# Performance work log

Hardware: AMD Instinct MI355X
Metric: run time of the kernel (lower is better)

Reference implementation:

```python
import jax, jax.numpy as jnp
import numpy as np

IN_DIM = 256
QK_DIM = IN_DIM // 8


def setup_inputs() -> dict:
    key = jax.random.key(0)
    ks = jax.random.split(key, 7)
    B, C, H, W = 4, IN_DIM, 64, 64
    s = 0.05
    return {
        "x": jax.random.normal(ks[0], (B, C, H, W), dtype=jnp.float32),
        "Wq": jax.random.normal(ks[1], (QK_DIM, C), dtype=jnp.float32) * s,
        "bq": jnp.zeros((QK_DIM,), dtype=jnp.float32),
        "Wk": jax.random.normal(ks[2], (QK_DIM, C), dtype=jnp.float32) * s,
        "bk": jnp.zeros((QK_DIM,), dtype=jnp.float32),
        "Wv": jax.random.normal(ks[3], (C, C), dtype=jnp.float32) * s,
        "bv": jnp.zeros((C,), dtype=jnp.float32),
        "gamma": jnp.zeros((1,), dtype=jnp.float32),
    }


def reference(x, Wq, bq, Wk, bk, Wv, bv, gamma):
    B, C, H, W = x.shape
    N = H * W
    xf = x.reshape(B, C, N)  # [B, C, N]
    # 1x1 convs are channel matmuls
    q = jnp.einsum('oc,bcn->bno', Wq, xf) + bq  # [B, N, Cqk]
    k = jnp.einsum('oc,bcn->bon', Wk, xf) + bk[None, :, None]  # [B, Cqk, N]
    energy = jnp.einsum('bno,bom->bnm', q, k)  # [B, N, N]
    attn = jax.nn.softmax(energy, axis=-1)
    v = jnp.einsum('oc,bcn->bon', Wv, xf) + bv[None, :, None]  # [B, C, N]
    # torch: out = bmm(v, attn^T) -> out[b,c,m] = sum_n v[b,c,n]*attn[m,n]
    out = jnp.einsum('bcn,bmn->bcm', v, attn)
    out = out.reshape(B, C, H, W)
    return gamma[0] * out + x
```

## Files before the change

kernel.cpp:

```cpp
#include <hip/hip_runtime.h>
#include <hip/hip_bf16.h>
#include <cstddef>

#define NB  4
#define NC  256
#define NN  4096
#define DQK 32
#define MT  64
#define JT  64
#define NIT (NN / JT)
#define PSTR 72
#define XSTR 40

typedef __attribute__((ext_vector_type(8))) short short8;
typedef __attribute__((ext_vector_type(4))) float f32x4;

#define MFMA16(a, b, c) __builtin_amdgcn_mfma_f32_16x16x32_bf16((a), (b), (c), 0, 0, 0)

__device__ inline unsigned pk2bf(float a, float b) {
  __hip_bfloat162 h = __float22bfloat162_rn(make_float2(a, b));
  unsigned u;
  __builtin_memcpy(&u, &h, 4);
  return u;
}

__global__ __launch_bounds__(256) void wcvt_kernel(
    const float* __restrict__ Wq, const float* __restrict__ Wk,
    const float* __restrict__ Wv, __hip_bfloat16* __restrict__ W16) {
  const int id4 = (blockIdx.x * 256 + threadIdx.x) * 4;
  const int row = id4 >> 8, col = id4 & 255;
  const float* src = (row < 32) ? Wq + row * 256
                   : (row < 64) ? Wk + (row - 32) * 256
                                : Wv + (row - 64) * 256;
  float4 vv = *(const float4*)(src + col);
  *(uint2*)(W16 + id4) = make_uint2(pk2bf(vv.x, vv.y), pk2bf(vv.z, vv.w));
}

__global__ __launch_bounds__(256) void proj_kernel(
    const float* __restrict__ x, const __hip_bfloat16* __restrict__ W16,
    const float* __restrict__ bq, const float* __restrict__ bk,
    const float* __restrict__ bv, __hip_bfloat16* __restrict__ q,
    __hip_bfloat16* __restrict__ kT, __hip_bfloat16* __restrict__ v) {
  __shared__ __hip_bfloat16 Xs[32 * XSTR];
  const int t = threadIdx.x;
  const int b = blockIdx.y, n0 = blockIdx.x * 32;
  const int w = __builtin_amdgcn_readfirstlane(t >> 6);
  const int ln = t & 15, quad = (t & 63) >> 4;
  const int sn = t & 31, scg = t >> 5;

  f32x4 zero4 = {0.f, 0.f, 0.f, 0.f};
  f32x4 acc[5][2];
#pragma unroll
  for (int i = 0; i < 5; ++i)
#pragma unroll
    for (int j = 0; j < 2; ++j) acc[i][j] = zero4;

  const float* xsrc = x + (size_t)b * NC * NN + n0 + sn;
  float xr[4];
#pragma unroll
  for (int i = 0; i < 4; ++i) xr[i] = xsrc[(size_t)(scg * 4 + i) * NN];

  for (int k0 = 0; k0 < NC; k0 += 32) {
    const unsigned px0 = pk2bf(xr[0], xr[1]);
    const unsigned px1 = pk2bf(xr[2], xr[3]);
    __syncthreads();
    *(uint2*)&Xs[sn * XSTR + scg * 4] = make_uint2(px0, px1);
    __syncthreads();
    const int kn = k0 + 32;
    if (kn < NC) {
#pragma unroll
      for (int i = 0; i < 4; ++i) xr[i] = xsrc[(size_t)(kn + scg * 4 + i) * NN];
    }
    short8 af[5], bfr[2];
#pragma unroll
    for (int ot = 0; ot < 5; ++ot)
      af[ot] = *(const short8*)(W16 + (size_t)(w * 80 + ot * 16 + ln) * NC + k0 + quad * 8);
#pragma unroll
    for (int nt = 0; nt < 2; ++nt)
      bfr[nt] = *(const short8*)&Xs[(nt * 16 + ln) * XSTR + quad * 8];
#pragma unroll
    for (int ot = 0; ot < 5; ++ot)
#pragma unroll
      for (int nt = 0; nt < 2; ++nt)
        acc[ot][nt] = MFMA16(af[ot], bfr[nt], acc[ot][nt]);
  }

#pragma unroll
  for (int ot = 0; ot < 5; ++ot) {
    const int gbase = w * 80 + ot * 16;
    if (gbase < 32) {
#pragma unroll
      for (int nt = 0; nt < 2; ++nt)
#pragma unroll
        for (int r = 0; r < 4; ++r) {
          const int row = gbase + quad * 4 + r;
          q[((size_t)b * NN + n0 + nt * 16 + ln) * DQK + row] =
              __hip_bfloat16(acc[ot][nt][r] + bq[row]);
        }
    } else if (gbase < 64) {
#pragma unroll
      for (int nt = 0; nt < 2; ++nt)
#pragma unroll
        for (int r = 0; r < 4; ++r) {
          const int row = gbase - 32 + quad * 4 + r;
          kT[((size_t)b * NN + n0 + nt * 16 + ln) * DQK + row] =
              __hip_bfloat16(acc[ot][nt][r] + bk[row]);
        }
    } else {
#pragma unroll
      for (int nt = 0; nt < 2; ++nt)
#pragma unroll
        for (int r = 0; r < 4; ++r) {
          const int c = gbase - 64 + quad * 4 + r;
          v[((size_t)b * NC + c) * NN + n0 + nt * 16 + ln] =
              __hip_bfloat16(acc[ot][nt][r] + bv[c]);
        }
    }
  }
}

__global__ __launch_bounds__(512, 2) void flash_kernel(
    const __hip_bfloat16* __restrict__ q, const __hip_bfloat16* __restrict__ kt,
    const __hip_bfloat16* __restrict__ v, const float* __restrict__ x,
    const float* __restrict__ gamma, float* __restrict__ out) {
  __shared__ __hip_bfloat16 Ps[2][MT * PSTR];
  __shared__ float arow[2][MT];
  __shared__ float lrow[MT];

  const int t  = threadIdx.x;
  const int bi = blockIdx.x;
  const int b  = (bi & 7) >> 1;
  const int m0 = (((bi & 1) * 32) + (bi >> 3)) * MT;

  const int w    = __builtin_amdgcn_readfirstlane(t >> 6);
  const int ln   = t & 15;
  const int quad = (t & 63) >> 4;

  const __hip_bfloat16* kb_base = kt + (size_t)b * NN * DQK;
  const __hip_bfloat16* v_base  = v + (size_t)b * NC * NN;

  if (w < 4) {
    const short8 qa =
        *(const short8*)(q + ((size_t)b * NN + m0 + w * 16 + ln) * DQK + quad * 8);
    float mreg[4], lreg[4];
#pragma unroll
    for (int r = 0; r < 4; ++r) { mreg[r] = -3.0e38f; lreg[r] = 0.f; }

    f32x4 zero4 = {0.f, 0.f, 0.f, 0.f};
    short8 kb[4];
#pragma unroll
    for (int jt = 0; jt < 4; ++jt)
      kb[jt] = *(const short8*)(kb_base + (size_t)(jt * 16 + ln) * DQK + quad * 8);

    for (int it = 0; it < NIT; ++it) {
      f32x4 sf[4];
#pragma unroll
      for (int jt = 0; jt < 4; ++jt) sf[jt] = MFMA16(qa, kb[jt], zero4);

      if (it + 1 < NIT) {
        const int jn = (it + 1) * JT;
#pragma unroll
        for (int jt = 0; jt < 4; ++jt)
          kb[jt] = *(const short8*)(kb_base + (size_t)(jn + jt * 16 + ln) * DQK + quad * 8);
      }

      float rmax[4];
#pragma unroll
      for (int r = 0; r < 4; ++r)
        rmax[r] = fmaxf(fmaxf(sf[0][r], sf[1][r]), fmaxf(sf[2][r], sf[3][r]));
#pragma unroll
      for (int off = 1; off < 16; off <<= 1)
#pragma unroll
        for (int r = 0; r < 4; ++r)
          rmax[r] = fmaxf(rmax[r], __shfl_xor(rmax[r], off));
      float alpha[4];
#pragma unroll
      for (int r = 0; r < 4; ++r) {
        const float mn = fmaxf(mreg[r], rmax[r]);
        alpha[r] = __expf(mreg[r] - mn);
        mreg[r] = mn;
      }
      float e[4][4], rsum[4];
#pragma unroll
      for (int r = 0; r < 4; ++r) rsum[r] = 0.f;
#pragma unroll
      for (int jt = 0; jt < 4; ++jt)
#pragma unroll
        for (int r = 0; r < 4; ++r) {
          e[jt][r] = __expf(sf[jt][r] - mreg[r]);
          rsum[r] += e[jt][r];
        }
#pragma unroll
      for (int off = 1; off < 16; off <<= 1)
#pragma unroll
        for (int r = 0; r < 4; ++r) rsum[r] += __shfl_xor(rsum[r], off);
#pragma unroll
      for (int r = 0; r < 4; ++r) lreg[r] = lreg[r] * alpha[r] + rsum[r];

      const int buf = it & 1;
#pragma unroll
      for (int jt = 0; jt < 4; ++jt)
#pragma unroll
        for (int r = 0; r < 4; ++r)
          Ps[buf][(w * 16 + quad * 4 + r) * PSTR + jt * 16 + ln] = __hip_bfloat16(e[jt][r]);
      if (ln == 0) {
#pragma unroll
        for (int r = 0; r < 4; ++r) arow[buf][w * 16 + quad * 4 + r] = alpha[r];
      }
      __syncthreads();
    }
    if (ln == 0) {
#pragma unroll
      for (int r = 0; r < 4; ++r) lrow[w * 16 + quad * 4 + r] = lreg[r];
    }
    __syncthreads();
  } else {
    const int c0 = (w - 4) * 64;
    f32x4 zero4 = {0.f, 0.f, 0.f, 0.f};
    f32x4 acc[4][4];
#pragma unroll
    for (int ct = 0; ct < 4; ++ct)
#pragma unroll
      for (int mt = 0; mt < 4; ++mt) acc[ct][mt] = zero4;

    short8 va[4][2];
#pragma unroll
    for (int ct = 0; ct < 4; ++ct)
#pragma unroll
      for (int ks = 0; ks < 2; ++ks)
        va[ct][ks] = *(const short8*)(v_base +
            (size_t)(c0 + ct * 16 + ln) * NN + ks * 32 + quad * 8);
    __syncthreads();

    for (int it = 1; it < NIT; ++it) {
      const int pbuf = (it - 1) & 1;
      float av[4];
#pragma unroll
      for (int mt = 0; mt < 4; ++mt) av[mt] = arow[pbuf][mt * 16 + ln];
#pragma unroll
      for (int ct = 0; ct < 4; ++ct)
#pragma unroll
        for (int mt = 0; mt < 4; ++mt) acc[ct][mt] *= av[mt];

#pragma unroll
      for (int ks = 0; ks < 2; ++ks) {
        short8 pb[4];
#pragma unroll
        for (int mt = 0; mt < 4; ++mt)
          pb[mt] = *(const short8*)&Ps[pbuf][(mt * 16 + ln) * PSTR + ks * 32 + quad * 8];
#pragma unroll
        for (int ct = 0; ct < 4; ++ct)
#pragma unroll
          for (int mt = 0; mt < 4; ++mt)
            acc[ct][mt] = MFMA16(va[ct][ks], pb[mt], acc[ct][mt]);
      }

      const int j0 = it * JT;
#pragma unroll
      for (int ct = 0; ct < 4; ++ct)
#pragma unroll
        for (int ks = 0; ks < 2; ++ks)
          va[ct][ks] = *(const short8*)(v_base +
              (size_t)(c0 + ct * 16 + ln) * NN + j0 + ks * 32 + quad * 8);
      __syncthreads();
    }

    {
      const int pbuf = (NIT - 1) & 1;
      float av[4];
#pragma unroll
      for (int mt = 0; mt < 4; ++mt) av[mt] = arow[pbuf][mt * 16 + ln];
#pragma unroll
      for (int ct = 0; ct < 4; ++ct)
#pragma unroll
        for (int mt = 0; mt < 4; ++mt) acc[ct][mt] *= av[mt];
#pragma unroll
      for (int ks = 0; ks < 2; ++ks) {
        short8 pb[4];
#pragma unroll
        for (int mt = 0; mt < 4; ++mt)
          pb[mt] = *(const short8*)&Ps[pbuf][(mt * 16 + ln) * PSTR + ks * 32 + quad * 8];
#pragma unroll
        for (int ct = 0; ct < 4; ++ct)
#pragma unroll
          for (int mt = 0; mt < 4; ++mt)
            acc[ct][mt] = MFMA16(va[ct][ks], pb[mt], acc[ct][mt]);
      }
    }
    __syncthreads();

    const float g0 = gamma[0];
    float li[4];
#pragma unroll
    for (int mt = 0; mt < 4; ++mt) li[mt] = 1.f / lrow[mt * 16 + ln];
#pragma unroll
    for (int ct = 0; ct < 4; ++ct)
#pragma unroll
      for (int r = 0; r < 4; ++r) {
        const int c = c0 + ct * 16 + quad * 4 + r;
        const float* xr = x + ((size_t)b * NC + c) * NN + m0;
        float* orow = out + ((size_t)b * NC + c) * NN + m0;
#pragma unroll
        for (int mt = 0; mt < 4; ++mt) {
          const int m = mt * 16 + ln;
          orow[m] = g0 * (acc[ct][mt][r] * li[mt]) + xr[m];
        }
      }
  }
}

extern "C" void kernel_launch(void* const* d_in, const int* in_sizes, int n_in,
                              void* d_out, int out_size, void* d_ws, size_t ws_size,
                              hipStream_t stream) {
  const float* x     = (const float*)d_in[0];
  const float* Wq    = (const float*)d_in[1];
  const float* bq    = (const float*)d_in[2];
  const float* Wk    = (const float*)d_in[3];
  const float* bk    = (const float*)d_in[4];
  const float* Wv    = (const float*)d_in[5];
  const float* bv    = (const float*)d_in[6];
  const float* gamma = (const float*)d_in[7];
  float* out = (float*)d_out;

  char* wsp = (char*)d_ws;
  __hip_bfloat16* W16 = (__hip_bfloat16*)wsp;  wsp += (size_t)320 * NC * 2;
  __hip_bfloat16* q   = (__hip_bfloat16*)wsp;  wsp += (size_t)NB * NN * DQK * 2;
  __hip_bfloat16* kT  = (__hip_bfloat16*)wsp;  wsp += (size_t)NB * NN * DQK * 2;
  __hip_bfloat16* v   = (__hip_bfloat16*)wsp;

  wcvt_kernel<<<dim3(80), dim3(256), 0, stream>>>(Wq, Wk, Wv, W16);
  proj_kernel<<<dim3(NN / 32, NB), dim3(256), 0, stream>>>(x, W16, bq, bk, bv, q, kT, v);
  flash_kernel<<<dim3(NB * NN / MT), dim3(512), 0, stream>>>(q, kT, v, x, gamma, out);
}
```

Before: 170.2 us.

## Halve flash query tile and replace MFMA projection with scalar fp32 kernels

Shrinks the flash-attention query tile from 64 to 32 rows and drops the block to 256 threads, with 2 softmax waves and 2 PV waves that each own 128 channels. This doubles the number of blocks, and each block now re-reads the full K and V for half as many queries. The bf16 weight-conversion kernel and the MFMA-based projection kernel are replaced by two scalar fp32 kernels, one for Q/K and one for V, which read the weights directly. The change trades projection-stage tensor-core use and V/K reuse for more parallelism in the attention stage.

Result: slower. 323.5 us (+90.1%).

```diff
diff --git a/kernel.cpp b/kernel.cpp
--- a/kernel.cpp
+++ b/kernel.cpp
@@ -6,11 +6,10 @@
 #define NC  256
 #define NN  4096
 #define DQK 32
-#define MT  64
+#define MT  32
 #define JT  64
 #define NIT (NN / JT)
 #define PSTR 72
-#define XSTR 40
 
 typedef __attribute__((ext_vector_type(8))) short short8;
 typedef __attribute__((ext_vector_type(4))) float f32x4;
@@ -24,102 +23,64 @@
   return u;
 }
 
-__global__ __launch_bounds__(256) void wcvt_kernel(
-    const float* __restrict__ Wq, const float* __restrict__ Wk,
-    const float* __restrict__ Wv, __hip_bfloat16* __restrict__ W16) {
-  const int id4 = (blockIdx.x * 256 + threadIdx.x) * 4;
-  const int row = id4 >> 8, col = id4 & 255;
-  const float* src = (row < 32) ? Wq + row * 256
-                   : (row < 64) ? Wk + (row - 32) * 256
-                                : Wv + (row - 64) * 256;
-  float4 vv = *(const float4*)(src + col);
-  *(uint2*)(W16 + id4) = make_uint2(pk2bf(vv.x, vv.y), pk2bf(vv.z, vv.w));
-}
-
-__global__ __launch_bounds__(256) void proj_kernel(
-    const float* __restrict__ x, const __hip_bfloat16* __restrict__ W16,
-    const float* __restrict__ bq, const float* __restrict__ bk,
-    const float* __restrict__ bv, __hip_bfloat16* __restrict__ q,
-    __hip_bfloat16* __restrict__ kT, __hip_bfloat16* __restrict__ v) {
-  __shared__ __hip_bfloat16 Xs[32 * XSTR];
+__global__ __launch_bounds__(256) void proj_qk_kernel(
+    const float* __restrict__ x, const float* __restrict__ Wq,
+    const float* __restrict__ bq, const float* __restrict__ Wk,
+    const float* __restrict__ bk, __hip_bfloat16* __restrict__ q,
+    __hip_bfloat16* __restrict__ kT) {
   const int t = threadIdx.x;
-  const int b = blockIdx.y, n0 = blockIdx.x * 32;
-  const int w = __builtin_amdgcn_readfirstlane(t >> 6);
-  const int ln = t & 15, quad = (t & 63) >> 4;
-  const int sn = t & 31, scg = t >> 5;
-
-  f32x4 zero4 = {0.f, 0.f, 0.f, 0.f};
-  f32x4 acc[5][2];
-#pragma unroll
-  for (int i = 0; i < 5; ++i)
-#pragma unroll
-    for (int j = 0; j < 2; ++j) acc[i][j] = zero4;
-
-  const float* xsrc = x + (size_t)b * NC * NN + n0 + sn;
-  float xr[4];
-#pragma unroll
-  for (int i = 0; i < 4; ++i) xr[i] = xsrc[(size_t)(scg * 4 + i) * NN];
-
-  for (int k0 = 0; k0 < NC; k0 += 32) {
-    const unsigned px0 = pk2bf(xr[0], xr[1]);
-    const unsigned px1 = pk2bf(xr[2], xr[3]);
-    __syncthreads();
-    *(uint2*)&Xs[sn * XSTR + scg * 4] = make_uint2(px0, px1);
-    __syncthreads();
-    const int kn = k0 + 32;
-    if (kn < NC) {
-#pragma unroll
-      for (int i = 0; i < 4; ++i) xr[i] = xsrc[(size_t)(kn + scg * 4 + i) * NN];
-    }
-    short8 af[5], bfr[2];
-#pragma unroll
-    for (int ot = 0; ot < 5; ++ot)
-      af[ot] = *(const short8*)(W16 + (size_t)(w * 80 + ot * 16 + ln) * NC + k0 + quad * 8);
-#pragma unroll
-    for (int nt = 0; nt < 2; ++nt)
-      bfr[nt] = *(const short8*)&Xs[(nt * 16 + ln) * XSTR + quad * 8];
-#pragma unroll
-    for (int ot = 0; ot < 5; ++ot)
-#pragma unroll
-      for (int nt = 0; nt < 2; ++nt)
-        acc[ot][nt] = MFMA16(af[ot], bfr[nt], acc[ot][nt]);
+  const int b = blockIdx.y;
+  const int n = blockIdx.x * 64 + (t & 63);
+  const int g = __builtin_amdgcn_readfirstlane(t >> 6);
+  const float* W    = (g < 2) ? Wq : Wk;
+  const float* bias = (g < 2) ? bq : bk;
+  const int obase = (g & 1) * 16;
+
+  float acc[16];
+#pragma unroll
+  for (int i = 0; i < 16; ++i) acc[i] = bias[obase + i];
+
+  const float* xp = x + ((size_t)b * NC) * NN + n;
+#pragma unroll 4
+  for (int c = 0; c < NC; ++c) {
+    float xv = xp[(size_t)c * NN];
+#pragma unroll
+    for (int i = 0; i < 16; ++i) acc[i] += W[(obase + i) * NC + c] * xv;
   }
-
-#pragma unroll
-  for (int ot = 0; ot < 5; ++ot) {
-    const int gbase = w * 80 + ot * 16;
-    if (gbase < 32) {
-#pragma unroll
-      for (int nt = 0; nt < 2; ++nt)
-#pragma unroll
-        for (int r = 0; r < 4; ++r) {
-          const int row = gbase + quad * 4 + r;
-          q[((size_t)b * NN + n0 + nt * 16 + ln) * DQK + row] =
-              __hip_bfloat16(acc[ot][nt][r] + bq[row]);
-        }
-    } else if (gbase < 64) {
-#pragma unroll
-      for (int nt = 0; nt < 2; ++nt)
-#pragma unroll
-        for (int r = 0; r < 4; ++r) {
-          const int row = gbase - 32 + quad * 4 + r;
-          kT[((size_t)b * NN + n0 + nt * 16 + ln) * DQK + row] =
-              __hip_bfloat16(acc[ot][nt][r] + bk[row]);
-        }
-    } else {
-#pragma unroll
-      for (int nt = 0; nt < 2; ++nt)
-#pragma unroll
-        for (int r = 0; r < 4; ++r) {
-          const int c = gbase - 64 + quad * 4 + r;
-          v[((size_t)b * NC + c) * NN + n0 + nt * 16 + ln] =
-              __hip_bfloat16(acc[ot][nt][r] + bv[c]);
-        }
-    }
+  __hip_bfloat16* dst = ((g < 2) ? q : kT) + ((size_t)b * NN + n) * DQK + obase;
+  unsigned p[8];
+#pragma unroll
+  for (int i = 0; i < 8; ++i) p[i] = pk2bf(acc[2 * i], acc[2 * i + 1]);
+  ((uint4*)dst)[0] = make_uint4(p[0], p[1], p[2], p[3]);
+  ((uint4*)dst)[1] = make_uint4(p[4], p[5], p[6], p[7]);
+}
+
+__global__ __launch_bounds__(256) void proj_v_kernel(
+    const float* __restrict__ x, const float* __restrict__ Wv,
+    const float* __restrict__ bv, __hip_bfloat16* __restrict__ v) {
+  const int t = threadIdx.x;
+  const int b = blockIdx.z;
+  const int n = blockIdx.x * 64 + (t & 63);
+  const int g = __builtin_amdgcn_readfirstlane(t >> 6);
+  const int obase = blockIdx.y * 128 + g * 32;
+
+  float acc[32];
+#pragma unroll
+  for (int i = 0; i < 32; ++i) acc[i] = bv[obase + i];
+
+  const float* xp = x + ((size_t)b * NC) * NN + n;
+#pragma unroll 2
+  for (int c = 0; c < NC; ++c) {
+    float xv = xp[(size_t)c * NN];
+#pragma unroll
+    for (int i = 0; i < 32; ++i) acc[i] += Wv[(obase + i) * NC + c] * xv;
   }
-}
-
-__global__ __launch_bounds__(512, 2) void flash_kernel(
+#pragma unroll
+  for (int i = 0; i < 32; ++i)
+    v[((size_t)b * NC + obase + i) * NN + n] = __hip_bfloat16(acc[i]);
+}
+
+__global__ __launch_bounds__(256, 2) void flash_kernel(
     const __hip_bfloat16* __restrict__ q, const __hip_bfloat16* __restrict__ kt,
     const __hip_bfloat16* __restrict__ v, const float* __restrict__ x,
     const float* __restrict__ gamma, float* __restrict__ out) {
@@ -130,7 +91,7 @@
   const int t  = threadIdx.x;
   const int bi = blockIdx.x;
   const int b  = (bi & 7) >> 1;
-  const int m0 = (((bi & 1) * 32) + (bi >> 3)) * MT;
+  const int m0 = (((bi & 1) * 64) + (bi >> 3)) * MT;
 
   const int w    = __builtin_amdgcn_readfirstlane(t >> 6);
   const int ln   = t & 15;
@@ -139,7 +100,7 @@
   const __hip_bfloat16* kb_base = kt + (size_t)b * NN * DQK;
   const __hip_bfloat16* v_base  = v + (size_t)b * NC * NN;
 
-  if (w < 4) {
+  if (w < 2) {
     const short8 qa =
         *(const short8*)(q + ((size_t)b * NN + m0 + w * 16 + ln) * DQK + quad * 8);
     float mreg[4], lreg[4];
@@ -215,17 +176,17 @@
     }
     __syncthreads();
   } else {
-    const int c0 = (w - 4) * 64;
+    const int c0 = (w - 2) * 128;
     f32x4 zero4 = {0.f, 0.f, 0.f, 0.f};
-    f32x4 acc[4][4];
-#pragma unroll
-    for (int ct = 0; ct < 4; ++ct)
-#pragma unroll
-      for (int mt = 0; mt < 4; ++mt) acc[ct][mt] = zero4;
-
-    short8 va[4][2];
-#pragma unroll
-    for (int ct = 0; ct < 4; ++ct)
+    f32x4 acc[8][2];
+#pragma unroll
+    for (int ct = 0; ct < 8; ++ct)
+#pragma unroll
+      for (int mt = 0; mt < 2; ++mt) acc[ct][mt] = zero4;
+
+    short8 va[8][2];
+#pragma unroll
+    for (int ct = 0; ct < 8; ++ct)
 #pragma unroll
       for (int ks = 0; ks < 2; ++ks)
         va[ct][ks] = *(const short8*)(v_base +
@@ -234,30 +195,30 @@
 
     for (int it = 1; it < NIT; ++it) {
       const int pbuf = (it - 1) & 1;
-      float av[4];
-#pragma unroll
-      for (int mt = 0; mt < 4; ++mt) av[mt] = arow[pbuf][mt * 16 + ln];
-#pragma unroll
-      for (int ct = 0; ct < 4; ++ct)
-#pragma unroll
-        for (int mt = 0; mt < 4; ++mt) acc[ct][mt] *= av[mt];
+      float av[2];
+#pragma unroll
+      for (int mt = 0; mt < 2; ++mt) av[mt] = arow[pbuf][mt * 16 + ln];
+#pragma unroll
+      for (int ct = 0; ct < 8; ++ct)
+#pragma unroll
+        for (int mt = 0; mt < 2; ++mt) acc[ct][mt] *= av[mt];
 
 #pragma unroll
       for (int ks = 0; ks < 2; ++ks) {
-        short8 pb[4];
-#pragma unroll
-        for (int mt = 0; mt < 4; ++mt)
+        short8 pb[2];
+#pragma unroll
+        for (int mt = 0; mt < 2; ++mt)
           pb[mt] = *(const short8*)&Ps[pbuf][(mt * 16 + ln) * PSTR + ks * 32 + quad * 8];
 #pragma unroll
-        for (int ct = 0; ct < 4; ++ct)
-#pragma unroll
-          for (int mt = 0; mt < 4; ++mt)
+        for (int ct = 0; ct < 8; ++ct)
+#pragma unroll
+          for (int mt = 0; mt < 2; ++mt)
             acc[ct][mt] = MFMA16(va[ct][ks], pb[mt], acc[ct][mt]);
       }
 
       const int j0 = it * JT;
 #pragma unroll
-      for (int ct = 0; ct < 4; ++ct)
+      for (int ct = 0; ct < 8; ++ct)
 #pragma unroll
         for (int ks = 0; ks < 2; ++ks)
           va[ct][ks] = *(const short8*)(v_base +
@@ -267,41 +228,41 @@
 
     {
       const int pbuf = (NIT - 1) & 1;
-      float av[4];
-#pragma unroll
-      for (int mt = 0; mt < 4; ++mt) av[mt] = arow[pbuf][mt * 16 + ln];
-#pragma unroll
-      for (int ct = 0; ct < 4; ++ct)
-#pragma unroll
-        for (int mt = 0; mt < 4; ++mt) acc[ct][mt] *= av[mt];
+      float av[2];
+#pragma unroll
+      for (int mt = 0; mt < 2; ++mt) av[mt] = arow[pbuf][mt * 16 + ln];
+#pragma unroll
+      for (int ct = 0; ct < 8; ++ct)
+#pragma unroll
+        for (int mt = 0; mt < 2; ++mt) acc[ct][mt] *= av[mt];
 #pragma unroll
       for (int ks = 0; ks < 2; ++ks) {
-        short8 pb[4];
-#pragma unroll
-        for (int mt = 0; mt < 4; ++mt)
+        short8 pb[2];
+#pragma unroll
+        for (int mt = 0; mt < 2; ++mt)
           pb[mt] = *(const short8*)&Ps[pbuf][(mt * 16 + ln) * PSTR + ks * 32 + quad * 8];
 #pragma unroll
-        for (int ct = 0; ct < 4; ++ct)
-#pragma unroll
-          for (int mt = 0; mt < 4; ++mt)
+        for (int ct = 0; ct < 8; ++ct)
+#pragma unroll
+          for (int mt = 0; mt < 2; ++mt)
             acc[ct][mt] = MFMA16(va[ct][ks], pb[mt], acc[ct][mt]);
       }
     }
     __syncthreads();
 
     const float g0 = gamma[0];
-    float li[4];
-#pragma unroll
-    for (int mt = 0; mt < 4; ++mt) li[mt] = 1.f / lrow[mt * 16 + ln];
-#pragma unroll
-    for (int ct = 0; ct < 4; ++ct)
+    float li[2];
+#pragma unroll
+    for (int mt = 0; mt < 2; ++mt) li[mt] = 1.f / lrow[mt * 16 + ln];
+#pragma unroll
+    for (int ct = 0; ct < 8; ++ct)
 #pragma unroll
       for (int r = 0; r < 4; ++r) {
         const int c = c0 + ct * 16 + quad * 4 + r;
         const float* xr = x + ((size_t)b * NC + c) * NN + m0;
         float* orow = out + ((size_t)b * NC + c) * NN + m0;
 #pragma unroll
-        for (int mt = 0; mt < 4; ++mt) {
+        for (int mt = 0; mt < 2; ++mt) {
           const int m = mt * 16 + ln;
           orow[m] = g0 * (acc[ct][mt][r] * li[mt]) + xr[m];
         }
@@ -322,13 +283,11 @@
   const float* gamma = (const float*)d_in[7];
   float* out = (float*)d_out;
 
-  char* wsp = (char*)d_ws;
-  __hip_bfloat16* W16 = (__hip_bfloat16*)wsp;  wsp += (size_t)320 * NC * 2;
-  __hip_bfloat16* q   = (__hip_bfloat16*)wsp;  wsp += (size_t)NB * NN * DQK * 2;
-  __hip_bfloat16* kT  = (__hip_bfloat16*)wsp;  wsp += (size_t)NB * NN * DQK * 2;
-  __hip_bfloat16* v   = (__hip_bfloat16*)wsp;
-
-  wcvt_kernel<<<dim3(80), dim3(256), 0, stream>>>(Wq, Wk, Wv, W16);
-  proj_kernel<<<dim3(NN / 32, NB), dim3(256), 0, stream>>>(x, W16, bq, bk, bv, q, kT, v);
-  flash_kernel<<<dim3(NB * NN / MT), dim3(512), 0, stream>>>(q, kT, v, x, gamma, out);
-}
+  __hip_bfloat16* q  = (__hip_bfloat16*)d_ws;
+  __hip_bfloat16* kT = q  + (size_t)NB * NN * DQK;
+  __hip_bfloat16* v  = kT + (size_t)NB * NN * DQK;
+
+  proj_qk_kernel<<<dim3(NN / 64, NB), dim3(256), 0, stream>>>(x, Wq, bq, Wk, bk, q, kT);
+  proj_v_kernel<<<dim3(NN / 64, 2, NB), dim3(256), 0, stream>>>(x, Wv, bv, v);
+  flash_kernel<<<dim3(NB * NN / MT), dim3(256), 0, stream>>>(q, kT, v, x, gamma, out);
+}
```

## Replace MFMA projection with fp32 scalar proj kernels and double flash key tile

Applied to the files above, without the earlier changes.

Drops the weight-conversion kernel and the bf16 MFMA projection, replacing them with two fp32 scalar-FMA projection kernels (one for q/k, one for v). Each splits the channel reduction across two wave groups and combines the halves through shared memory. In the flash kernel the key tile grows from 64 to 128, halving the number of iterations and barriers, and V loads are interleaved per k-slice. The trade-off is more registers and shared memory in flash, plus a scalar-FMA projection that may be slower than the MFMA version and rereads x for each output group.

After: 235.9 us. 38.6% more time.

```diff
diff --git a/kernel.cpp b/kernel.cpp
--- a/kernel.cpp
+++ b/kernel.cpp
@@ -7,10 +7,9 @@
 #define NN  4096
 #define DQK 32
 #define MT  64
-#define JT  64
+#define JT  128
 #define NIT (NN / JT)
-#define PSTR 72
-#define XSTR 40
+#define PSTR 140
 
 typedef __attribute__((ext_vector_type(8))) short short8;
 typedef __attribute__((ext_vector_type(4))) float f32x4;
@@ -24,97 +23,112 @@
   return u;
 }
 
-__global__ __launch_bounds__(256) void wcvt_kernel(
-    const float* __restrict__ Wq, const float* __restrict__ Wk,
-    const float* __restrict__ Wv, __hip_bfloat16* __restrict__ W16) {
-  const int id4 = (blockIdx.x * 256 + threadIdx.x) * 4;
-  const int row = id4 >> 8, col = id4 & 255;
-  const float* src = (row < 32) ? Wq + row * 256
-                   : (row < 64) ? Wk + (row - 32) * 256
-                                : Wv + (row - 64) * 256;
-  float4 vv = *(const float4*)(src + col);
-  *(uint2*)(W16 + id4) = make_uint2(pk2bf(vv.x, vv.y), pk2bf(vv.z, vv.w));
-}
-
-__global__ __launch_bounds__(256) void proj_kernel(
-    const float* __restrict__ x, const __hip_bfloat16* __restrict__ W16,
-    const float* __restrict__ bq, const float* __restrict__ bk,
-    const float* __restrict__ bv, __hip_bfloat16* __restrict__ q,
-    __hip_bfloat16* __restrict__ kT, __hip_bfloat16* __restrict__ v) {
-  __shared__ __hip_bfloat16 Xs[32 * XSTR];
+__global__ __launch_bounds__(512) void proj_qk_kernel(
+    const float* __restrict__ x, const float* __restrict__ Wq,
+    const float* __restrict__ bq, const float* __restrict__ Wk,
+    const float* __restrict__ bk, __hip_bfloat16* __restrict__ q,
+    __hip_bfloat16* __restrict__ kT) {
+  __shared__ float Rs[256 * 17];
   const int t = threadIdx.x;
-  const int b = blockIdx.y, n0 = blockIdx.x * 32;
+  const int b = blockIdx.y;
+  const int n = blockIdx.x * 64 + (t & 63);
   const int w = __builtin_amdgcn_readfirstlane(t >> 6);
-  const int ln = t & 15, quad = (t & 63) >> 4;
-  const int sn = t & 31, scg = t >> 5;
-
-  f32x4 zero4 = {0.f, 0.f, 0.f, 0.f};
-  f32x4 acc[5][2];
-#pragma unroll
-  for (int i = 0; i < 5; ++i)
-#pragma unroll
-    for (int j = 0; j < 2; ++j) acc[i][j] = zero4;
-
-  const float* xsrc = x + (size_t)b * NC * NN + n0 + sn;
-  float xr[4];
-#pragma unroll
-  for (int i = 0; i < 4; ++i) xr[i] = xsrc[(size_t)(scg * 4 + i) * NN];
-
-  for (int k0 = 0; k0 < NC; k0 += 32) {
-    const unsigned px0 = pk2bf(xr[0], xr[1]);
-    const unsigned px1 = pk2bf(xr[2], xr[3]);
-    __syncthreads();
-    *(uint2*)&Xs[sn * XSTR + scg * 4] = make_uint2(px0, px1);
-    __syncthreads();
-    const int kn = k0 + 32;
-    if (kn < NC) {
-#pragma unroll
-      for (int i = 0; i < 4; ++i) xr[i] = xsrc[(size_t)(kn + scg * 4 + i) * NN];
-    }
-    short8 af[5], bfr[2];
-#pragma unroll
-    for (int ot = 0; ot < 5; ++ot)
-      af[ot] = *(const short8*)(W16 + (size_t)(w * 80 + ot * 16 + ln) * NC + k0 + quad * 8);
-#pragma unroll
-    for (int nt = 0; nt < 2; ++nt)
-      bfr[nt] = *(const short8*)&Xs[(nt * 16 + ln) * XSTR + quad * 8];
-#pragma unroll
-    for (int ot = 0; ot < 5; ++ot)
-#pragma unroll
-      for (int nt = 0; nt < 2; ++nt)
-        acc[ot][nt] = MFMA16(af[ot], bfr[nt], acc[ot][nt]);
-  }
-
-#pragma unroll
-  for (int ot = 0; ot < 5; ++ot) {
-    const int gbase = w * 80 + ot * 16;
-    if (gbase < 32) {
-#pragma unroll
-      for (int nt = 0; nt < 2; ++nt)
-#pragma unroll
-        for (int r = 0; r < 4; ++r) {
-          const int row = gbase + quad * 4 + r;
-          q[((size_t)b * NN + n0 + nt * 16 + ln) * DQK + row] =
-              __hip_bfloat16(acc[ot][nt][r] + bq[row]);
-        }
-    } else if (gbase < 64) {
-#pragma unroll
-      for (int nt = 0; nt < 2; ++nt)
-#pragma unroll
-        for (int r = 0; r < 4; ++r) {
-          const int row = gbase - 32 + quad * 4 + r;
-          kT[((size_t)b * NN + n0 + nt * 16 + ln) * DQK + row] =
-              __hip_bfloat16(acc[ot][nt][r] + bk[row]);
-        }
-    } else {
-#pragma unroll
-      for (int nt = 0; nt < 2; ++nt)
-#pragma unroll
-        for (int r = 0; r < 4; ++r) {
-          const int c = gbase - 64 + quad * 4 + r;
-          v[((size_t)b * NC + c) * NN + n0 + nt * 16 + ln] =
-              __hip_bfloat16(acc[ot][nt][r] + bv[c]);
-        }
+  const int g = w & 3;
+  const int ch = w >> 2;
+  const float* W    = (g < 2) ? Wq : Wk;
+  const int obase = (g & 1) * 16;
+
+  float acc[16];
+#pragma unroll
+  for (int i = 0; i < 16; ++i) acc[i] = 0.f;
+
+  const float* xp = x + ((size_t)b * NC + ch * 128) * NN + n;
+  const float* Wp = W + obase * NC + ch * 128;
+
+  float xv[8];
+#pragma unroll
+  for (int i = 0; i < 8; ++i) xv[i] = xp[(size_t)i * NN];
+  for (int cc = 0; cc < 128; cc += 8) {
+    float xn[8];
+    if (cc + 8 < 128) {
+#pragma unroll
+      for (int i = 0; i < 8; ++i) xn[i] = xp[(size_t)(cc + 8 + i) * NN];
+    }
+#pragma unroll
+    for (int i = 0; i < 8; ++i)
+#pragma unroll
+      for (int o = 0; o < 16; ++o) acc[o] += Wp[o * NC + cc + i] * xv[i];
+#pragma unroll
+    for (int i = 0; i < 8; ++i) xv[i] = xn[i];
+  }
+
+  if (w >= 4) {
+    const int tl = t - 256;
+#pragma unroll
+    for (int i = 0; i < 16; ++i) Rs[tl * 17 + i] = acc[i];
+  }
+  __syncthreads();
+  if (w < 4) {
+    const float* bias = (g < 2) ? bq : bk;
+#pragma unroll
+    for (int i = 0; i < 16; ++i) acc[i] += Rs[t * 17 + i] + bias[obase + i];
+    __hip_bfloat16* dst = ((g < 2) ? q : kT) + ((size_t)b * NN + n) * DQK + obase;
+    unsigned p[8];
+#pragma unroll
+    for (int i = 0; i < 8; ++i) p[i] = pk2bf(acc[2 * i], acc[2 * i + 1]);
+    ((uint4*)dst)[0] = make_uint4(p[0], p[1], p[2], p[3]);
+    ((uint4*)dst)[1] = make_uint4(p[4], p[5], p[6], p[7]);
+  }
+}
+
+__global__ __launch_bounds__(512) void proj_v_kernel(
+    const float* __restrict__ x, const float* __restrict__ Wv,
+    const float* __restrict__ bv, __hip_bfloat16* __restrict__ v) {
+  __shared__ float Rs[256 * 17];
+  const int t = threadIdx.x;
+  const int b = blockIdx.z;
+  const int n = blockIdx.x * 64 + (t & 63);
+  const int w = __builtin_amdgcn_readfirstlane(t >> 6);
+  const int g = w & 3;
+  const int ch = w >> 2;
+  const int obase = blockIdx.y * 64 + g * 16;
+
+  float acc[16];
+#pragma unroll
+  for (int i = 0; i < 16; ++i) acc[i] = 0.f;
+
+  const float* xp = x + ((size_t)b * NC + ch * 128) * NN + n;
+  const float* Wp = Wv + obase * NC + ch * 128;
+
+  float xv[8];
+#pragma unroll
+  for (int i = 0; i < 8; ++i) xv[i] = xp[(size_t)i * NN];
+  for (int cc = 0; cc < 128; cc += 8) {
+    float xn[8];
+    if (cc + 8 < 128) {
+#pragma unroll
+      for (int i = 0; i < 8; ++i) xn[i] = xp[(size_t)(cc + 8 + i) * NN];
+    }
+#pragma unroll
+    for (int i = 0; i < 8; ++i)
+#pragma unroll
+      for (int o = 0; o < 16; ++o) acc[o] += Wp[o * NC + cc + i] * xv[i];
+#pragma unroll
+    for (int i = 0; i < 8; ++i) xv[i] = xn[i];
+  }
+
+  if (w >= 4) {
+    const int tl = t - 256;
+#pragma unroll
+    for (int i = 0; i < 16; ++i) Rs[tl * 17 + i] = acc[i];
+  }
+  __syncthreads();
+  if (w < 4) {
+#pragma unroll
+    for (int i = 0; i < 16; ++i) {
+      const int c = obase + i;
+      v[((size_t)b * NC + c) * NN + n] =
+          __hip_bfloat16(acc[i] + Rs[t * 17 + i] + bv[c]);
     }
   }
 }
@@ -147,27 +161,30 @@
     for (int r = 0; r < 4; ++r) { mreg[r] = -3.0e38f; lreg[r] = 0.f; }
 
     f32x4 zero4 = {0.f, 0.f, 0.f, 0.f};
-    short8 kb[4];
-#pragma unroll
-    for (int jt = 0; jt < 4; ++jt)
+    short8 kb[8];
+#pragma unroll
+    for (int jt = 0; jt < 8; ++jt)
       kb[jt] = *(const short8*)(kb_base + (size_t)(jt * 16 + ln) * DQK + quad * 8);
 
     for (int it = 0; it < NIT; ++it) {
-      f32x4 sf[4];
-#pragma unroll
-      for (int jt = 0; jt < 4; ++jt) sf[jt] = MFMA16(qa, kb[jt], zero4);
+      f32x4 sf[8];
+#pragma unroll
+      for (int jt = 0; jt < 8; ++jt) sf[jt] = MFMA16(qa, kb[jt], zero4);
 
       if (it + 1 < NIT) {
         const int jn = (it + 1) * JT;
 #pragma unroll
-        for (int jt = 0; jt < 4; ++jt)
+        for (int jt = 0; jt < 8; ++jt)
           kb[jt] = *(const short8*)(kb_base + (size_t)(jn + jt * 16 + ln) * DQK + quad * 8);
       }
 
       float rmax[4];
 #pragma unroll
-      for (int r = 0; r < 4; ++r)
-        rmax[r] = fmaxf(fmaxf(sf[0][r], sf[1][r]), fmaxf(sf[2][r], sf[3][r]));
+      for (int r = 0; r < 4; ++r) {
+        float a0 = fmaxf(fmaxf(sf[0][r], sf[1][r]), fmaxf(sf[2][r], sf[3][r]));
+        float a1 = fmaxf(fmaxf(sf[4][r], sf[5][r]), fmaxf(sf[6][r], sf[7][r]));
+        rmax[r] = fmaxf(a0, a1);
+      }
 #pragma unroll
       for (int off = 1; off < 16; off <<= 1)
 #pragma unroll
@@ -180,11 +197,11 @@
         alpha[r] = __expf(mreg[r] - mn);
         mreg[r] = mn;
       }
-      float e[4][4], rsum[4];
+      float e[8][4], rsum[4];
 #pragma unroll
       for (int r = 0; r < 4; ++r) rsum[r] = 0.f;
 #pragma unroll
-      for (int jt = 0; jt < 4; ++jt)
+      for (int jt = 0; jt < 8; ++jt)
 #pragma unroll
         for (int r = 0; r < 4; ++r) {
           e[jt][r] = __expf(sf[jt][r] - mreg[r]);
@@ -199,7 +216,7 @@
 
       const int buf = it & 1;
 #pragma unroll
-      for (int jt = 0; jt < 4; ++jt)
+      for (int jt = 0; jt < 8; ++jt)
 #pragma unroll
         for (int r = 0; r < 4; ++r)
           Ps[buf][(w * 16 + quad * 4 + r) * PSTR + jt * 16 + ln] = __hip_bfloat16(e[jt][r]);
@@ -223,11 +240,11 @@
 #pragma unroll
       for (int mt = 0; mt < 4; ++mt) acc[ct][mt] = zero4;
 
-    short8 va[4][2];
+    short8 va[4][4];
 #pragma unroll
     for (int ct = 0; ct < 4; ++ct)
 #pragma unroll
-      for (int ks = 0; ks < 2; ++ks)
+      for (int ks = 0; ks < 4; ++ks)
         va[ct][ks] = *(const short8*)(v_base +
             (size_t)(c0 + ct * 16 + ln) * NN + ks * 32 + quad * 8);
     __syncthreads();
@@ -242,8 +259,9 @@
 #pragma unroll
         for (int mt = 0; mt < 4; ++mt) acc[ct][mt] *= av[mt];
 
-#pragma unroll
-      for (int ks = 0; ks < 2; ++ks) {
+      const int j0 = it * JT;
+#pragma unroll
+      for (int ks = 0; ks < 4; ++ks) {
         short8 pb[4];
 #pragma unroll
         for (int mt = 0; mt < 4; ++mt)
@@ -253,15 +271,11 @@
 #pragma unroll
           for (int mt = 0; mt < 4; ++mt)
             acc[ct][mt] = MFMA16(va[ct][ks], pb[mt], acc[ct][mt]);
-      }
-
-      const int j0 = it * JT;
-#pragma unroll
-      for (int ct = 0; ct < 4; ++ct)
-#pragma unroll
-        for (int ks = 0; ks < 2; ++ks)
+#pragma unroll
+        for (int ct = 0; ct < 4; ++ct)
           va[ct][ks] = *(const short8*)(v_base +
               (size_t)(c0 + ct * 16 + ln) * NN + j0 + ks * 32 + quad * 8);
+      }
       __syncthreads();
     }
 
@@ -275,7 +289,7 @@
 #pragma unroll
         for (int mt = 0; mt < 4; ++mt) acc[ct][mt] *= av[mt];
 #pragma unroll
-      for (int ks = 0; ks < 2; ++ks) {
+      for (int ks = 0; ks < 4; ++ks) {
         short8 pb[4];
 #pragma unroll
         for (int mt = 0; mt < 4; ++mt)
@@ -322,13 +336,11 @@
   const float* gamma = (const float*)d_in[7];
   float* out = (float*)d_out;
 
-  char* wsp = (char*)d_ws;
-  __hip_bfloat16* W16 = (__hip_bfloat16*)wsp;  wsp += (size_t)320 * NC * 2;
-  __hip_bfloat16* q   = (__hip_bfloat16*)wsp;  wsp += (size_t)NB * NN * DQK * 2;
-  __hip_bfloat16* kT  = (__hip_bfloat16*)wsp;  wsp += (size_t)NB * NN * DQK * 2;
-  __hip_bfloat16* v   = (__hip_bfloat16*)wsp;
-
-  wcvt_kernel<<<dim3(80), dim3(256), 0, stream>>>(Wq, Wk, Wv, W16);
-  proj_kernel<<<dim3(NN / 32, NB), dim3(256), 0, stream>>>(x, W16, bq, bk, bv, q, kT, v);
+  __hip_bfloat16* q  = (__hip_bfloat16*)d_ws;
+  __hip_bfloat16* kT = q  + (size_t)NB * NN * DQK;
+  __hip_bfloat16* v  = kT + (size_t)NB * NN * DQK;
+
+  proj_qk_kernel<<<dim3(NN / 64, NB), dim3(512), 0, stream>>>(x, Wq, bq, Wk, bk, q, kT);
+  proj_v_kernel<<<dim3(NN / 64, 4, NB), dim3(512), 0, stream>>>(x, Wv, bv, v);
   flash_kernel<<<dim3(NB * NN / MT), dim3(512), 0, stream>>>(q, kT, v, x, gamma, out);
 }
```
